# Kernel tuning notes

Measured on AMD Instinct MI355X. Metric: run time of the kernel, lower is better.

Reference implementation:

```python
import jax, jax.numpy as jnp
import numpy as np

N = 50000
E = 1600000
EPS = 1e-8  # torch CosineSimilarity eps


def gcn_layer(x, W, b, edge_index, n):
    src, dst = edge_index[0], edge_index[1]
    h = x @ W  # [n, out]
    deg = jnp.ones((n,), x.dtype).at[dst].add(1.0)  # in-degree + self loop
    dinv = jax.lax.rsqrt(deg)
    norm = dinv[src] * dinv[dst]  # [E]
    agg = jnp.zeros_like(h).at[dst].add(norm[:, None] * h[src])
    agg = agg + (dinv * dinv)[:, None] * h  # self-loop term (norm = dinv_i^2)
    return agg + b


def setup_inputs() -> dict:
    key = jax.random.key(0)
    ks = jax.random.split(key, 12)
    drug = jax.random.normal(ks[0], (N, 2048), jnp.float32)
    target = jax.random.normal(ks[1], (N, 1024), jnp.float32)
    drug_edge_index = jax.random.randint(ks[2], (2, E), 0, N)
    target_edge_index = jax.random.randint(ks[3], (2, E), 0, N)
    # projector weights (xavier-ish scale), stored as [in, out]
    Wd = jax.random.normal(ks[4], (2048, 1024), jnp.float32) * np.sqrt(2.0 / (2048 + 1024))
    bd = jnp.zeros((1024,), jnp.float32)
    Wt = jax.random.normal(ks[5], (1024, 1024), jnp.float32) * np.sqrt(2.0 / (1024 + 1024))
    bt = jnp.zeros((1024,), jnp.float32)
    # shared GCN layers (applied to both graphs)
    W1 = jax.random.normal(ks[6], (1024, 512), jnp.float32) * np.sqrt(2.0 / (1024 + 512))
    b1 = jnp.zeros((512,), jnp.float32)
    W2 = jax.random.normal(ks[7], (512, 512), jnp.float32) * np.sqrt(2.0 / (512 + 512))
    b2 = jnp.zeros((512,), jnp.float32)
    return {"drug": drug, "target": target,
            "drug_edge_index": drug_edge_index, "target_edge_index": target_edge_index,
            "Wd": Wd, "bd": bd, "Wt": Wt, "bt": bt,
            "W1": W1, "b1": b1, "W2": W2, "b2": b2}


def reference(drug, target, drug_edge_index, target_edge_index,
              Wd, bd, Wt, bt, W1, b1, W2, b2):
    # projectors: Linear + ReLU
    dp = jax.nn.relu(drug @ Wd + bd)   # [N, 1024]
    tp = jax.nn.relu(target @ Wt + bt)  # [N, 1024]
    # shared GNN layers on each graph
    dp = gcn_layer(dp, W1, b1, drug_edge_index, N)
    tp = gcn_layer(tp, W1, b1, target_edge_index, N)
    dp = gcn_layer(dp, W2, b2, drug_edge_index, N)
    tp = gcn_layer(tp, W2, b2, target_edge_index, N)
    # Cosine similarity along feature dim, then sigmoid
    dn = jnp.maximum(jnp.linalg.norm(dp, axis=1), EPS)
    tn = jnp.maximum(jnp.linalg.norm(tp, axis=1), EPS)
    cos = jnp.sum(dp * tp, axis=1) / (dn * tn)  # [N]
    return jax.nn.sigmoid(cos)
```

## Files before the change

kernel.cpp:

```cpp
#include <hip/hip_runtime.h>
#include <math.h>

#define NNODES 50000
#define NEDGES 1600000
#define MP 50048

typedef unsigned int uint_t;
typedef __attribute__((ext_vector_type(8))) short short8;
typedef __attribute__((ext_vector_type(4))) float f32x4;

__device__ __forceinline__ unsigned short f2bf(float f){
  union { float f; uint_t u; } v; v.f = f;
  uint_t u = v.u;
  uint_t r = (u + 0x7fffu + ((u >> 16) & 1u)) >> 16;
  return (unsigned short)r;
}
__device__ __forceinline__ float bf2f(uint_t u){
  union { uint_t u; float f; } v; v.u = u << 16;
  return v.f;
}

__global__ void k_init_counts(int* cnt_d, int* cnt_t, int n){
  int i = blockIdx.x*blockDim.x + threadIdx.x;
  if (i < n){ cnt_d[i] = 0; cnt_t[i] = 0; }
}

__global__ void k_count(const int* __restrict__ ei, int* __restrict__ cnt, int e){
  int i = blockIdx.x*blockDim.x + threadIdx.x;
  if (i < e) atomicAdd(&cnt[ei[e + i]], 1);
}

__global__ __launch_bounds__(1024) void k_scan_blk(
    const int* __restrict__ cnt_d, const int* __restrict__ cnt_t,
    int* __restrict__ rp_d, int* __restrict__ rp_t,
    float* __restrict__ dinv_d, float* __restrict__ dinv_t,
    int* __restrict__ bsum, int n)
{
  const int g = blockIdx.y;
  const int* cnt = g ? cnt_t : cnt_d;
  int* rp        = g ? rp_t  : rp_d;
  float* dinv    = g ? dinv_t: dinv_d;
  __shared__ int sdata[1024];
  const int tid = threadIdx.x;
  const int i = blockIdx.x*1024 + tid;
  int v = (i < n) ? cnt[i] : 0;
  sdata[tid] = v;
  __syncthreads();
  for (int off = 1; off < 1024; off <<= 1){
    int t = (tid >= off) ? sdata[tid - off] : 0;
    __syncthreads();
    sdata[tid] += t;
    __syncthreads();
  }
  if (i < n){
    rp[i]   = sdata[tid] - v;
    dinv[i] = 1.0f / sqrtf(1.0f + (float)v);
  }
  if (tid == 1023) bsum[g*64 + blockIdx.x] = sdata[1023];
}

__global__ __launch_bounds__(128) void k_scan_bsum(
    int* __restrict__ bsum, int* __restrict__ rp_d, int* __restrict__ rp_t,
    int nb, int n)
{
  const int g = threadIdx.x >> 6;
  const int lane = threadIdx.x & 63;
  int orig = (lane < nb) ? bsum[g*64 + lane] : 0;
  int v = orig;
  #pragma unroll
  for (int off = 1; off < 64; off <<= 1){
    int t = __shfl_up(v, off);
    if (lane >= off) v += t;
  }
  if (lane < nb) bsum[g*64 + lane] = v - orig;
  if (lane == nb-1){
    if (g) rp_t[n] = v; else rp_d[n] = v;
  }
}

__global__ __launch_bounds__(1024) void k_scan_add(
    const int* __restrict__ bsum,
    int* __restrict__ rp_d, int* __restrict__ rp_t,
    int* __restrict__ cur_d, int* __restrict__ cur_t, int n)
{
  const int g = blockIdx.y;
  int* rp  = g ? rp_t  : rp_d;
  int* cur = g ? cur_t : cur_d;
  const int i = blockIdx.x*1024 + threadIdx.x;
  if (i < n){
    int v = rp[i] + bsum[g*64 + blockIdx.x];
    rp[i] = v;
    cur[i] = v;
  }
}

__global__ void k_fill(const int* __restrict__ ei, int* __restrict__ cur,
                       int* __restrict__ col, float* __restrict__ w,
                       const float* __restrict__ dinv, int e){
  int i = blockIdx.x*blockDim.x + threadIdx.x;
  if (i < e){
    int src = ei[i], dst = ei[e + i];
    int pos = atomicAdd(&cur[dst], 1);
    col[pos] = src;
    w[pos]   = dinv[src];
  }
}

__global__ void k_cast_bf(const float* __restrict__ src, unsigned short* __restrict__ dst,
                          long long n_src, long long n_total){
  long long i = ((long long)blockIdx.x * 256 + threadIdx.x) * 4;
  if (i >= n_total) return;
  ushort4 o;
  if (i < n_src){
    float4 v = *(const float4*)&src[i];
    o.x = f2bf(v.x); o.y = f2bf(v.y); o.z = f2bf(v.z); o.w = f2bf(v.w);
  } else { o.x = 0; o.y = 0; o.z = 0; o.w = 0; }
  *(ushort4*)&dst[i] = o;
}

__global__ __launch_bounds__(256) void k_tr_cast(const float* __restrict__ W,
    unsigned short* __restrict__ WT, int K, int N){
  __shared__ float t[32][33];
  int bx = blockIdx.x * 32;
  int by = blockIdx.y * 32;
  int x = threadIdx.x & 31, y0 = threadIdx.x >> 5;
  for (int y = y0; y < 32; y += 8)
    t[y][x] = W[(size_t)(by + y)*N + bx + x];
  __syncthreads();
  for (int y = y0; y < 32; y += 8)
    WT[(size_t)(bx + y)*K + by + x] = f2bf(t[x][y]);
}

__global__ __launch_bounds__(256) void gemm_bf16(
    const unsigned short* __restrict__ A, const unsigned short* __restrict__ BT,
    const float* __restrict__ bias, void* __restrict__ Cv,
    int N, int K, int relu, int out_bf16)
{
  __shared__ unsigned short As[128*32];
  __shared__ unsigned short Bs[128*32];
  const int tid  = threadIdx.x;
  const int lane = tid & 63;
  const int wave = tid >> 6;

  const int gx  = gridDim.x;
  const int nwg = gx * gridDim.y;
  const int id  = blockIdx.y * gx + blockIdx.x;
  const int q = nwg >> 3, r = nwg & 7;
  const int xcd = id & 7, rank = id >> 3;
  const int nid = (xcd < r) ? (xcd*(q+1) + rank)
                            : (r*(q+1) + (xcd - r)*q + rank);
  const long long bm = (long long)(nid / gx) * 128;
  const int bn = (nid % gx) * 128;

  const int wm = (wave & 1) * 64;
  const int wn = (wave >> 1) * 64;
  const int srow = lane >> 2;
  const int sg   = lane & 3;
  const int gcol = (sg ^ ((srow >> 1) & 3)) * 8;
  const unsigned short* pa0 = A  + (bm + wave*32 + srow) * K + gcol;
  const unsigned short* pb0 = BT + (long long)(bn + wave*32 + srow) * K + gcol;
  unsigned short* lA0 = As + (wave*32     )*32;
  unsigned short* lA1 = As + (wave*32 + 16)*32;
  unsigned short* lB0 = Bs + (wave*32     )*32;
  unsigned short* lB1 = Bs + (wave*32 + 16)*32;

  const int lm = lane & 15;
  const int q2 = lane >> 4;
  const int fcol = ((q2 ^ ((lm >> 1) & 3)) * 8);

  f32x4 acc[4][4] = {};

  for (int k0 = 0; k0 < K; k0 += 32){
    __builtin_amdgcn_global_load_lds((const __attribute__((address_space(1))) void*)(pa0 + k0),
        (__attribute__((address_space(3))) void*)lA0, 16, 0, 0);
    __builtin_amdgcn_global_load_lds((const __attribute__((address_space(1))) void*)(pa0 + 16*K + k0),
        (__attribute__((address_space(3))) void*)lA1, 16, 0, 0);
    __builtin_amdgcn_global_load_lds((const __attribute__((address_space(1))) void*)(pb0 + k0),
        (__attribute__((address_space(3))) void*)lB0, 16, 0, 0);
    __builtin_amdgcn_global_load_lds((const __attribute__((address_space(1))) void*)(pb0 + 16*K + k0),
        (__attribute__((address_space(3))) void*)lB1, 16, 0, 0);
    __syncthreads();
    short8 af[4], bfr[4];
    #pragma unroll
    for (int i = 0; i < 4; i++){
      af[i]  = *(const short8*)&As[(wm + 16*i + lm)*32 + fcol];
      bfr[i] = *(const short8*)&Bs[(wn + 16*i + lm)*32 + fcol];
    }
    #pragma unroll
    for (int i = 0; i < 4; i++)
      #pragma unroll
      for (int j = 0; j < 4; j++)
        acc[i][j] = __builtin_amdgcn_mfma_f32_16x16x32_bf16(af[i], bfr[j], acc[i][j], 0, 0, 0);
    __syncthreads();
  }

  #pragma unroll
  for (int j = 0; j < 4; j++){
    int c = bn + wn + 16*j + lm;
    float bv = bias ? bias[c] : 0.f;
    #pragma unroll
    for (int i = 0; i < 4; i++){
      long long mrow = bm + wm + 16*i + q2*4;
      #pragma unroll
      for (int rr = 0; rr < 4; rr++){
        float v = acc[i][j][rr] + bv;
        if (relu) v = fmaxf(v, 0.f);
        if (out_bf16) ((unsigned short*)Cv)[(mrow + rr)*N + c] = f2bf(v);
        else          ((float*)Cv)[(mrow + rr)*N + c] = v;
      }
    }
  }
}

__global__ __launch_bounds__(256) void k_agg_bf(
    const unsigned short* __restrict__ H, const int* __restrict__ rowptr,
    const int* __restrict__ col, const float* __restrict__ w,
    const float* __restrict__ dinv, const float* __restrict__ bias,
    unsigned short* __restrict__ out, int nrows)
{
  const int half = threadIdx.x >> 7;
  const int t    = threadIdx.x & 127;
  const int row  = blockIdx.x*2 + half;
  if (row >= nrows) return;
  const int f = t * 4;
  const int beg = rowptr[row], end = rowptr[row+1];
  float a0 = 0.f, a1 = 0.f, a2 = 0.f, a3 = 0.f;
  int e = beg;
  for (; e + 3 < end; e += 4){
    int s0 = col[e], s1 = col[e+1], s2 = col[e+2], s3 = col[e+3];
    float w0 = w[e], w1 = w[e+1], w2 = w[e+2], w3 = w[e+3];
    uint2 h0 = *(const uint2*)&H[(size_t)s0*512 + f];
    uint2 h1 = *(const uint2*)&H[(size_t)s1*512 + f];
    uint2 h2 = *(const uint2*)&H[(size_t)s2*512 + f];
    uint2 h3 = *(const uint2*)&H[(size_t)s3*512 + f];
    a0 += w0*bf2f(h0.x & 0xffffu) + w1*bf2f(h1.x & 0xffffu)
        + w2*bf2f(h2.x & 0xffffu) + w3*bf2f(h3.x & 0xffffu);
    a1 += w0*bf2f(h0.x >> 16)     + w1*bf2f(h1.x >> 16)
        + w2*bf2f(h2.x >> 16)     + w3*bf2f(h3.x >> 16);
    a2 += w0*bf2f(h0.y & 0xffffu) + w1*bf2f(h1.y & 0xffffu)
        + w2*bf2f(h2.y & 0xffffu) + w3*bf2f(h3.y & 0xffffu);
    a3 += w0*bf2f(h0.y >> 16)     + w1*bf2f(h1.y >> 16)
        + w2*bf2f(h2.y >> 16)     + w3*bf2f(h3.y >> 16);
  }
  for (; e < end; ++e){
    int s = col[e]; float ws = w[e];
    uint2 h = *(const uint2*)&H[(size_t)s*512 + f];
    a0 += ws*bf2f(h.x & 0xffffu); a1 += ws*bf2f(h.x >> 16);
    a2 += ws*bf2f(h.y & 0xffffu); a3 += ws*bf2f(h.y >> 16);
  }
  float di = dinv[row];
  float sc = di*di;
  uint2 hs = *(const uint2*)&H[(size_t)row*512 + f];
  float4 bv = *(const float4*)&bias[f];
  float o0 = di*a0 + sc*bf2f(hs.x & 0xffffu) + bv.x;
  float o1 = di*a1 + sc*bf2f(hs.x >> 16)     + bv.y;
  float o2 = di*a2 + sc*bf2f(hs.y & 0xffffu) + bv.z;
  float o3 = di*a3 + sc*bf2f(hs.y >> 16)     + bv.w;
  uint2 o;
  o.x = (uint_t)f2bf(o0) | ((uint_t)f2bf(o1) << 16);
  o.y = (uint_t)f2bf(o2) | ((uint_t)f2bf(o3) << 16);
  *(uint2*)&out[(size_t)row*512 + f] = o;
}

__global__ __launch_bounds__(256) void k_cos_bf(const unsigned short* __restrict__ a,
    const unsigned short* __restrict__ b, float* __restrict__ out, int n)
{
  const int lane = threadIdx.x & 63;
  const int wid  = threadIdx.x >> 6;
  const int row  = blockIdx.x*4 + wid;
  if (row >= n) return;
  uint4 x = *(const uint4*)&a[(size_t)row*512 + lane*8];
  uint4 y = *(const uint4*)&b[(size_t)row*512 + lane*8];
  uint_t xs[4] = {x.x, x.y, x.z, x.w};
  uint_t ys[4] = {y.x, y.y, y.z, y.w};
  float dot = 0.f, na = 0.f, nb = 0.f;
  #pragma unroll
  for (int k = 0; k < 4; k++){
    float x0 = bf2f(xs[k] & 0xffffu), x1 = bf2f(xs[k] >> 16);
    float y0 = bf2f(ys[k] & 0xffffu), y1 = bf2f(ys[k] >> 16);
    dot += x0*y0 + x1*y1;
    na  += x0*x0 + x1*x1;
    nb  += y0*y0 + y1*y1;
  }
  #pragma unroll
  for (int off = 32; off; off >>= 1){
    dot += __shfl_down(dot, off);
    na  += __shfl_down(na , off);
    nb  += __shfl_down(nb , off);
  }
  if (lane == 0){
    float dn = fmaxf(sqrtf(na), 1e-8f);
    float tn = fmaxf(sqrtf(nb), 1e-8f);
    out[row] = 1.f/(1.f + expf(-dot/(dn*tn)));
  }
}

extern "C" void kernel_launch(void* const* d_in, const int* in_sizes, int n_in,
                              void* d_out, int out_size, void* d_ws, size_t ws_size,
                              hipStream_t stream)
{
  (void)in_sizes; (void)n_in; (void)out_size; (void)ws_size;
  const float* drug   = (const float*)d_in[0];
  const float* target = (const float*)d_in[1];
  const int*   ei_d   = (const int*)d_in[2];
  const int*   ei_t   = (const int*)d_in[3];
  const float* Wd = (const float*)d_in[4];
  const float* bd = (const float*)d_in[5];
  const float* Wt = (const float*)d_in[6];
  const float* bt = (const float*)d_in[7];
  const float* W1 = (const float*)d_in[8];
  const float* b1 = (const float*)d_in[9];
  const float* W2 = (const float*)d_in[10];
  const float* b2 = (const float*)d_in[11];
  float* out = (float*)d_out;

  const int n = NNODES, E = NEDGES;
  char* ws = (char*)d_ws;
  size_t off = 0;
  auto alloc = [&](size_t bytes)->char* {
    char* p = ws + off; off += (bytes + 255) & ~(size_t)255; return p;
  };
  int*   cnt_d  = (int*)  alloc((size_t)n*4);
  int*   cnt_t  = (int*)  alloc((size_t)n*4);
  int*   rp_d   = (int*)  alloc((size_t)(n+1)*4);
  int*   rp_t   = (int*)  alloc((size_t)(n+1)*4);
  int*   cur_d  = (int*)  alloc((size_t)n*4);
  int*   cur_t  = (int*)  alloc((size_t)n*4);
  int*   col_d  = (int*)  alloc((size_t)E*4);
  int*   col_t  = (int*)  alloc((size_t)E*4);
  float* w_d    = (float*)alloc((size_t)E*4);
  float* w_t    = (float*)alloc((size_t)E*4);
  float* dinv_d = (float*)alloc((size_t)n*4);
  float* dinv_t = (float*)alloc((size_t)n*4);
  int*   bsum   = (int*)  alloc(128*4);
  unsigned short* WdT = (unsigned short*)alloc((size_t)1024*2048*2);
  unsigned short* WtT = (unsigned short*)alloc((size_t)1024*1024*2);
  unsigned short* W1T = (unsigned short*)alloc((size_t)512*1024*2);
  unsigned short* W2T = (unsigned short*)alloc((size_t)512*512*2);
  unsigned short* bufA = (unsigned short*)alloc((size_t)MP*2048*2);
  unsigned short* bufP = (unsigned short*)alloc((size_t)2*MP*1024*2);
  unsigned short* bufH = (unsigned short*)alloc((size_t)2*MP*512*2);
  unsigned short* dp1 = bufP;
  unsigned short* dp2 = bufA;

  dim3 blk(256);
  const int NB = (n + 1023)/1024;

  k_init_counts<<<(n+255)/256, blk, 0, stream>>>(cnt_d, cnt_t, n);
  k_count<<<(E+255)/256, blk, 0, stream>>>(ei_d, cnt_d, E);
  k_count<<<(E+255)/256, blk, 0, stream>>>(ei_t, cnt_t, E);
  k_scan_blk<<<dim3(NB,2), 1024, 0, stream>>>(cnt_d, cnt_t, rp_d, rp_t, dinv_d, dinv_t, bsum, n);
  k_scan_bsum<<<1, 128, 0, stream>>>(bsum, rp_d, rp_t, NB, n);
  k_scan_add<<<dim3(NB,2), 1024, 0, stream>>>(bsum, rp_d, rp_t, cur_d, cur_t, n);
  k_fill<<<(E+255)/256, blk, 0, stream>>>(ei_d, cur_d, col_d, w_d, dinv_d, E);
  k_fill<<<(E+255)/256, blk, 0, stream>>>(ei_t, cur_t, col_t, w_t, dinv_t, E);

  k_tr_cast<<<dim3(1024/32, 2048/32), blk, 0, stream>>>(Wd, WdT, 2048, 1024);
  k_tr_cast<<<dim3(1024/32, 1024/32), blk, 0, stream>>>(Wt, WtT, 1024, 1024);
  k_tr_cast<<<dim3( 512/32, 1024/32), blk, 0, stream>>>(W1, W1T, 1024,  512);
  k_tr_cast<<<dim3( 512/32,  512/32), blk, 0, stream>>>(W2, W2T,  512,  512);

  {
    long long nsrc = (long long)n*2048, ntot = (long long)MP*2048;
    k_cast_bf<<<(unsigned)((ntot/4 + 255)/256), blk, 0, stream>>>(drug, bufA, nsrc, ntot);
  }
  gemm_bf16<<<dim3(8, MP/128), blk, 0, stream>>>(bufA, WdT, bd, bufP, 1024, 2048, 1, 1);
  {
    long long nsrc = (long long)n*1024, ntot = (long long)MP*1024;
    k_cast_bf<<<(unsigned)((ntot/4 + 255)/256), blk, 0, stream>>>(target, bufA, nsrc, ntot);
  }
  gemm_bf16<<<dim3(8, MP/128), blk, 0, stream>>>(bufA, WtT, bt, bufP + (size_t)MP*1024, 1024, 1024, 1, 1);

  gemm_bf16<<<dim3(4, (2*MP)/128), blk, 0, stream>>>(bufP, W1T, nullptr, bufH, 512, 1024, 0, 1);
  k_agg_bf<<<(n+1)/2, blk, 0, stream>>>(bufH, rp_d, col_d, w_d, dinv_d, b1, dp1, n);
  k_agg_bf<<<(n+1)/2, blk, 0, stream>>>(bufH + (size_t)MP*512, rp_t, col_t, w_t, dinv_t, b1,
                                        dp1 + (size_t)MP*512, n);

  gemm_bf16<<<dim3(4, (2*MP)/128), blk, 0, stream>>>(dp1, W2T, nullptr, bufH, 512, 512, 0, 1);
  k_agg_bf<<<(n+1)/2, blk, 0, stream>>>(bufH, rp_d, col_d, w_d, dinv_d, b2, dp2, n);
  k_agg_bf<<<(n+1)/2, blk, 0, stream>>>(bufH + (size_t)MP*512, rp_t, col_t, w_t, dinv_t, b2,
                                        dp2 + (size_t)MP*512, n);

  k_cos_bf<<<(n+3)/4, blk, 0, stream>>>(dp2, dp2 + (size_t)MP*512, out, n);
}
```

Baseline: 2.757 ms.

## Use 256x256 GEMM tiles with 4-stage LDS pipeline and pack CSR col/weight

The bf16 GEMM moves from 128x128 tiles with 256 threads and a single LDS buffer to 256x256 tiles with 512 threads and a 4-deep ring of LDS buffers. Global-to-LDS loads are issued three K-steps ahead and gated with vmcnt waits, and MFMA runs at raised wave priority, so memory latency overlaps compute with one barrier per step. MP padding grows to a multiple of 256 to fit the new tile. Separately, the CSR column index and edge weight are packed into one int2 array so aggregation does a single 8-byte load per edge. The cost is 128 KB of LDS per block and more accumulator registers per wave, which limits occupancy.

```diff
diff --git a/kernel.cpp b/kernel.cpp
--- a/kernel.cpp
+++ b/kernel.cpp
@@ -3,7 +3,7 @@
 
 #define NNODES 50000
 #define NEDGES 1600000
-#define MP 50048
+#define MP 50176
 
 typedef unsigned int uint_t;
 typedef __attribute__((ext_vector_type(8))) short short8;
@@ -95,14 +95,12 @@
 }
 
 __global__ void k_fill(const int* __restrict__ ei, int* __restrict__ cur,
-                       int* __restrict__ col, float* __restrict__ w,
-                       const float* __restrict__ dinv, int e){
+                       int2* __restrict__ cw, const float* __restrict__ dinv, int e){
   int i = blockIdx.x*blockDim.x + threadIdx.x;
   if (i < e){
     int src = ei[i], dst = ei[e + i];
     int pos = atomicAdd(&cur[dst], 1);
-    col[pos] = src;
-    w[pos]   = dinv[src];
+    cw[pos] = make_int2(src, __float_as_int(dinv[src]));
   }
 }
 
@@ -131,16 +129,18 @@
     WT[(size_t)(bx + y)*K + by + x] = f2bf(t[x][y]);
 }
 
-__global__ __launch_bounds__(256) void gemm_bf16(
+__global__ __launch_bounds__(512, 2) void gemm_bf16(
     const unsigned short* __restrict__ A, const unsigned short* __restrict__ BT,
     const float* __restrict__ bias, void* __restrict__ Cv,
     int N, int K, int relu, int out_bf16)
 {
-  __shared__ unsigned short As[128*32];
-  __shared__ unsigned short Bs[128*32];
+  __shared__ unsigned short As[4][256*32];
+  __shared__ unsigned short Bs[4][256*32];
   const int tid  = threadIdx.x;
   const int lane = tid & 63;
   const int wave = tid >> 6;
+  const int wm   = wave >> 2;
+  const int wn   = wave & 3;
 
   const int gx  = gridDim.x;
   const int nwg = gx * gridDim.y;
@@ -149,58 +149,82 @@
   const int xcd = id & 7, rank = id >> 3;
   const int nid = (xcd < r) ? (xcd*(q+1) + rank)
                             : (r*(q+1) + (xcd - r)*q + rank);
-  const long long bm = (long long)(nid / gx) * 128;
-  const int bn = (nid % gx) * 128;
-
-  const int wm = (wave & 1) * 64;
-  const int wn = (wave >> 1) * 64;
+  const long long bm = (long long)(nid / gx) * 256;
+  const int bn = (nid % gx) * 256;
+
   const int srow = lane >> 2;
   const int sg   = lane & 3;
-  const int gcol = (sg ^ ((srow >> 1) & 3)) * 8;
-  const unsigned short* pa0 = A  + (bm + wave*32 + srow) * K + gcol;
-  const unsigned short* pb0 = BT + (long long)(bn + wave*32 + srow) * K + gcol;
-  unsigned short* lA0 = As + (wave*32     )*32;
-  unsigned short* lA1 = As + (wave*32 + 16)*32;
-  unsigned short* lB0 = Bs + (wave*32     )*32;
-  unsigned short* lB1 = Bs + (wave*32 + 16)*32;
+  const int gchunk = sg ^ ((srow >> 1) & 3);
+  const unsigned short* pa0 = A  + (bm + wave*32 +      srow) * K + gchunk*8;
+  const unsigned short* pa1 = A  + (bm + wave*32 + 16 + srow) * K + gchunk*8;
+  const unsigned short* pb0 = BT + ((long long)bn + wave*32 +      srow) * K + gchunk*8;
+  const unsigned short* pb1 = BT + ((long long)bn + wave*32 + 16 + srow) * K + gchunk*8;
+  const int ldA0 = (wave*32     ) * 32;
+  const int ldA1 = (wave*32 + 16) * 32;
+
+  auto STAGE = [&](int t_){
+    const int bi = t_ & 3;
+    const int k0 = t_ * 32;
+    __builtin_amdgcn_global_load_lds((const __attribute__((address_space(1))) void*)(pa0 + k0),
+        (__attribute__((address_space(3))) void*)&As[bi][ldA0], 16, 0, 0);
+    __builtin_amdgcn_global_load_lds((const __attribute__((address_space(1))) void*)(pa1 + k0),
+        (__attribute__((address_space(3))) void*)&As[bi][ldA1], 16, 0, 0);
+    __builtin_amdgcn_global_load_lds((const __attribute__((address_space(1))) void*)(pb0 + k0),
+        (__attribute__((address_space(3))) void*)&Bs[bi][ldA0], 16, 0, 0);
+    __builtin_amdgcn_global_load_lds((const __attribute__((address_space(1))) void*)(pb1 + k0),
+        (__attribute__((address_space(3))) void*)&Bs[bi][ldA1], 16, 0, 0);
+  };
 
   const int lm = lane & 15;
   const int q2 = lane >> 4;
-  const int fcol = ((q2 ^ ((lm >> 1) & 3)) * 8);
-
-  f32x4 acc[4][4] = {};
-
-  for (int k0 = 0; k0 < K; k0 += 32){
-    __builtin_amdgcn_global_load_lds((const __attribute__((address_space(1))) void*)(pa0 + k0),
-        (__attribute__((address_space(3))) void*)lA0, 16, 0, 0);
-    __builtin_amdgcn_global_load_lds((const __attribute__((address_space(1))) void*)(pa0 + 16*K + k0),
-        (__attribute__((address_space(3))) void*)lA1, 16, 0, 0);
-    __builtin_amdgcn_global_load_lds((const __attribute__((address_space(1))) void*)(pb0 + k0),
-        (__attribute__((address_space(3))) void*)lB0, 16, 0, 0);
-    __builtin_amdgcn_global_load_lds((const __attribute__((address_space(1))) void*)(pb0 + 16*K + k0),
-        (__attribute__((address_space(3))) void*)lB1, 16, 0, 0);
-    __syncthreads();
-    short8 af[4], bfr[4];
+  const int fcol = (q2 ^ ((lm >> 1) & 3)) * 8;
+
+  f32x4 acc[8][4] = {};
+
+  auto COMPUTE = [&](int t_){
+    const int bi = t_ & 3;
+    short8 af[8], bfr[4];
     #pragma unroll
-    for (int i = 0; i < 4; i++){
-      af[i]  = *(const short8*)&As[(wm + 16*i + lm)*32 + fcol];
-      bfr[i] = *(const short8*)&Bs[(wn + 16*i + lm)*32 + fcol];
-    }
+    for (int i = 0; i < 8; i++)
+      af[i]  = *(const short8*)&As[bi][(wm*128 + 16*i + lm)*32 + fcol];
     #pragma unroll
-    for (int i = 0; i < 4; i++)
+    for (int j = 0; j < 4; j++)
+      bfr[j] = *(const short8*)&Bs[bi][(wn*64  + 16*j + lm)*32 + fcol];
+    __builtin_amdgcn_s_setprio(1);
+    #pragma unroll
+    for (int i = 0; i < 8; i++)
       #pragma unroll
       for (int j = 0; j < 4; j++)
         acc[i][j] = __builtin_amdgcn_mfma_f32_16x16x32_bf16(af[i], bfr[j], acc[i][j], 0, 0, 0);
-    __syncthreads();
-  }
+    __builtin_amdgcn_s_setprio(0);
+  };
+
+  const int NT = K >> 5;
+  STAGE(0); STAGE(1); STAGE(2);
+
+  for (int t = 0; t < NT - 3; ++t){
+    asm volatile("s_waitcnt vmcnt(8)" ::: "memory");
+    __builtin_amdgcn_s_barrier();
+    STAGE(t + 3);
+    COMPUTE(t);
+  }
+  asm volatile("s_waitcnt vmcnt(8)" ::: "memory");
+  __builtin_amdgcn_s_barrier();
+  COMPUTE(NT - 3);
+  asm volatile("s_waitcnt vmcnt(4)" ::: "memory");
+  __builtin_amdgcn_s_barrier();
+  COMPUTE(NT - 2);
+  asm volatile("s_waitcnt vmcnt(0)" ::: "memory");
+  __builtin_amdgcn_s_barrier();
+  COMPUTE(NT - 1);
 
   #pragma unroll
   for (int j = 0; j < 4; j++){
-    int c = bn + wn + 16*j + lm;
+    int c = bn + wn*64 + 16*j + lm;
     float bv = bias ? bias[c] : 0.f;
     #pragma unroll
-    for (int i = 0; i < 4; i++){
-      long long mrow = bm + wm + 16*i + q2*4;
+    for (int i = 0; i < 8; i++){
+      long long mrow = bm + wm*128 + 16*i + q2*4;
       #pragma unroll
       for (int rr = 0; rr < 4; rr++){
         float v = acc[i][j][rr] + bv;
@@ -214,9 +238,8 @@
 
 __global__ __launch_bounds__(256) void k_agg_bf(
     const unsigned short* __restrict__ H, const int* __restrict__ rowptr,
-    const int* __restrict__ col, const float* __restrict__ w,
-    const float* __restrict__ dinv, const float* __restrict__ bias,
-    unsigned short* __restrict__ out, int nrows)
+    const int2* __restrict__ cw, const float* __restrict__ dinv,
+    const float* __restrict__ bias, unsigned short* __restrict__ out, int nrows)
 {
   const int half = threadIdx.x >> 7;
   const int t    = threadIdx.x & 127;
@@ -227,12 +250,13 @@
   float a0 = 0.f, a1 = 0.f, a2 = 0.f, a3 = 0.f;
   int e = beg;
   for (; e + 3 < end; e += 4){
-    int s0 = col[e], s1 = col[e+1], s2 = col[e+2], s3 = col[e+3];
-    float w0 = w[e], w1 = w[e+1], w2 = w[e+2], w3 = w[e+3];
-    uint2 h0 = *(const uint2*)&H[(size_t)s0*512 + f];
-    uint2 h1 = *(const uint2*)&H[(size_t)s1*512 + f];
-    uint2 h2 = *(const uint2*)&H[(size_t)s2*512 + f];
-    uint2 h3 = *(const uint2*)&H[(size_t)s3*512 + f];
+    int2 c0 = cw[e], c1 = cw[e+1], c2 = cw[e+2], c3 = cw[e+3];
+    float w0 = __int_as_float(c0.y), w1 = __int_as_float(c1.y);
+    float w2 = __int_as_float(c2.y), w3 = __int_as_float(c3.y);
+    uint2 h0 = *(const uint2*)&H[(size_t)c0.x*512 + f];
+    uint2 h1 = *(const uint2*)&H[(size_t)c1.x*512 + f];
+    uint2 h2 = *(const uint2*)&H[(size_t)c2.x*512 + f];
+    uint2 h3 = *(const uint2*)&H[(size_t)c3.x*512 + f];
     a0 += w0*bf2f(h0.x & 0xffffu) + w1*bf2f(h1.x & 0xffffu)
         + w2*bf2f(h2.x & 0xffffu) + w3*bf2f(h3.x & 0xffffu);
     a1 += w0*bf2f(h0.x >> 16)     + w1*bf2f(h1.x >> 16)
@@ -243,7 +267,8 @@
         + w2*bf2f(h2.y >> 16)     + w3*bf2f(h3.y >> 16);
   }
   for (; e < end; ++e){
-    int s = col[e]; float ws = w[e];
+    int2 ce = cw[e];
+    int s = ce.x; float ws = __int_as_float(ce.y);
     uint2 h = *(const uint2*)&H[(size_t)s*512 + f];
     a0 += ws*bf2f(h.x & 0xffffu); a1 += ws*bf2f(h.x >> 16);
     a2 += ws*bf2f(h.y & 0xffffu); a3 += ws*bf2f(h.y >> 16);
@@ -326,10 +351,8 @@
   int*   rp_t   = (int*)  alloc((size_t)(n+1)*4);
   int*   cur_d  = (int*)  alloc((size_t)n*4);
   int*   cur_t  = (int*)  alloc((size_t)n*4);
-  int*   col_d  = (int*)  alloc((size_t)E*4);
-  int*   col_t  = (int*)  alloc((size_t)E*4);
-  float* w_d    = (float*)alloc((size_t)E*4);
-  float* w_t    = (float*)alloc((size_t)E*4);
+  int2*  cw_d   = (int2*) alloc((size_t)E*8);
+  int2*  cw_t   = (int2*) alloc((size_t)E*8);
   float* dinv_d = (float*)alloc((size_t)n*4);
   float* dinv_t = (float*)alloc((size_t)n*4);
   int*   bsum   = (int*)  alloc(128*4);
@@ -352,8 +375,8 @@
   k_scan_blk<<<dim3(NB,2), 1024, 0, stream>>>(cnt_d, cnt_t, rp_d, rp_t, dinv_d, dinv_t, bsum, n);
   k_scan_bsum<<<1, 128, 0, stream>>>(bsum, rp_d, rp_t, NB, n);
   k_scan_add<<<dim3(NB,2), 1024, 0, stream>>>(bsum, rp_d, rp_t, cur_d, cur_t, n);
-  k_fill<<<(E+255)/256, blk, 0, stream>>>(ei_d, cur_d, col_d, w_d, dinv_d, E);
-  k_fill<<<(E+255)/256, blk, 0, stream>>>(ei_t, cur_t, col_t, w_t, dinv_t, E);
+  k_fill<<<(E+255)/256, blk, 0, stream>>>(ei_d, cur_d, cw_d, dinv_d, E);
+  k_fill<<<(E+255)/256, blk, 0, stream>>>(ei_t, cur_t, cw_t, dinv_t, E);
 
   k_tr_cast<<<dim3(1024/32, 2048/32), blk, 0, stream>>>(Wd, WdT, 2048, 1024);
   k_tr_cast<<<dim3(1024/32, 1024/32), blk, 0, stream>>>(Wt, WtT, 1024, 1024);
@@ -364,21 +387,21 @@
     long long nsrc = (long long)n*2048, ntot = (long long)MP*2048;
     k_cast_bf<<<(unsigned)((ntot/4 + 255)/256), blk, 0, stream>>>(drug, bufA, nsrc, ntot);
   }
-  gemm_bf16<<<dim3(8, MP/128), blk, 0, stream>>>(bufA, WdT, bd, bufP, 1024, 2048, 1, 1);
+  gemm_bf16<<<dim3(1024/256, MP/256), dim3(512), 0, stream>>>(bufA, WdT, bd, bufP, 1024, 2048, 1, 1);
   {
     long long nsrc = (long long)n*1024, ntot = (long long)MP*1024;
     k_cast_bf<<<(unsigned)((ntot/4 + 255)/256), blk, 0, stream>>>(target, bufA, nsrc, ntot);
   }
-  gemm_bf16<<<dim3(8, MP/128), blk, 0, stream>>>(bufA, WtT, bt, bufP + (size_t)MP*1024, 1024, 1024, 1, 1);
-
-  gemm_bf16<<<dim3(4, (2*MP)/128), blk, 0, stream>>>(bufP, W1T, nullptr, bufH, 512, 1024, 0, 1);
-  k_agg_bf<<<(n+1)/2, blk, 0, stream>>>(bufH, rp_d, col_d, w_d, dinv_d, b1, dp1, n);
-  k_agg_bf<<<(n+1)/2, blk, 0, stream>>>(bufH + (size_t)MP*512, rp_t, col_t, w_t, dinv_t, b1,
+  gemm_bf16<<<dim3(1024/256, MP/256), dim3(512), 0, stream>>>(bufA, WtT, bt, bufP + (size_t)MP*1024, 1024, 1024, 1, 1);
+
+  gemm_bf16<<<dim3(512/256, (2*MP)/256), dim3(512), 0, stream>>>(bufP, W1T, nullptr, bufH, 512, 1024, 0, 1);
+  k_agg_bf<<<(n+1)/2, blk, 0, stream>>>(bufH, rp_d, cw_d, dinv_d, b1, dp1, n);
+  k_agg_bf<<<(n+1)/2, blk, 0, stream>>>(bufH + (size_t)MP*512, rp_t, cw_t, dinv_t, b1,
                                         dp1 + (size_t)MP*512, n);
 
-  gemm_bf16<<<dim3(4, (2*MP)/128), blk, 0, stream>>>(dp1, W2T, nullptr, bufH, 512, 512, 0, 1);
-  k_agg_bf<<<(n+1)/2, blk, 0, stream>>>(bufH, rp_d, col_d, w_d, dinv_d, b2, dp2, n);
-  k_agg_bf<<<(n+1)/2, blk, 0, stream>>>(bufH + (size_t)MP*512, rp_t, col_t, w_t, dinv_t, b2,
+  gemm_bf16<<<dim3(512/256, (2*MP)/256), dim3(512), 0, stream>>>(dp1, W2T, nullptr, bufH, 512, 512, 0, 1);
+  k_agg_bf<<<(n+1)/2, blk, 0, stream>>>(bufH, rp_d, cw_d, dinv_d, b2, dp2, n);
+  k_agg_bf<<<(n+1)/2, blk, 0, stream>>>(bufH + (size_t)MP*512, rp_t, cw_t, dinv_t, b2,
                                         dp2 + (size_t)MP*512, n);
 
   k_cos_bf<<<(n+3)/4, blk, 0, stream>>>(dp2, dp2 + (size_t)MP*512, out, n);
```

Result: slower. 2.840 ms (+3.0%).
